# Kernel optimization log

Measured on AMD Instinct MI355X. Metric: run time of the kernel, lower is better.

Reference implementation:

```python
import jax, jax.numpy as jnp
import numpy as np

B, S, D = 1, 1024, 1024
NH, DH, DR = 8, 128, 64
DCQ, DC = 768, 256
INTER, E, TOPK = 512, 8, 2

def rmsnorm(x, w, eps=1e-6):
    return x * jax.lax.rsqrt(jnp.mean(x * x, -1, keepdims=True) + eps) * w

def lin(x, w, b):
    return x @ w.T + b

def apply_rope(x, cos, sin):
    # x: [b, s, h, d]; cos/sin: [S, d//2]; complex rotate pairs (even, odd)
    b, s, h, d = x.shape
    xr = x.reshape(b, s, h, d // 2, 2)
    x0, x1 = xr[..., 0], xr[..., 1]
    c = cos[None, :s, None, :]
    sn = sin[None, :s, None, :]
    return jnp.stack([x0 * c - x1 * sn, x0 * sn + x1 * c], -1).reshape(b, s, h, d)

def setup_inputs():
    keys = iter(jax.random.split(jax.random.key(0), 64))
    def nrm(*shape):
        return jax.random.normal(next(keys), shape, jnp.float32) * 0.02
    theta = 1.0 / (10000.0 ** (jnp.arange(0, DR, 2, dtype=jnp.float32) / DR))
    ang = jnp.arange(S, dtype=jnp.float32)[:, None] * theta[None, :]
    return dict(
        h=jax.random.normal(next(keys), (B, S, D), jnp.float32),
        freqs_cos=jnp.cos(ang), freqs_sin=jnp.sin(ang),
        mask=jnp.triu(jnp.ones((S, S), bool), 1),
        attn_norm_w=jnp.ones(D), ffn_norm_w=jnp.ones(D),
        wq_down=nrm(DCQ, D), bq_down=jnp.zeros(DCQ), q_norm_w=jnp.ones(DCQ),
        wqc=nrm(NH * DH, DCQ), bqc=jnp.zeros(NH * DH),
        wqr=nrm(NH * DR, DCQ), bqr=jnp.zeros(NH * DR),
        wkr=nrm(DR, D), bkr=jnp.zeros(DR), kr_norm_w=jnp.ones(DR),
        wkv_down=nrm(DC, D), bkv_down=jnp.zeros(DC), kv_norm_w=jnp.ones(DC),
        wkc=nrm(NH * DH, DC), bkc=jnp.zeros(NH * DH),
        wvc=nrm(NH * DH, DC), bvc=jnp.zeros(NH * DH),
        wo=nrm(D, NH * DH), bo=jnp.zeros(D),
        sw1=nrm(INTER, D), sb1=jnp.zeros(INTER), sw2=nrm(D, INTER), sb2=jnp.zeros(D),
        sw3=nrm(INTER, D), sb3=jnp.zeros(INTER),
        ew1=nrm(E, INTER, D), eb1=jnp.zeros((E, INTER)), ew2=nrm(E, D, INTER), eb2=jnp.zeros((E, D)),
        ew3=nrm(E, INTER, D), eb3=jnp.zeros((E, INTER)),
        centroids=jax.random.normal(next(keys), (E, D), jnp.float32), biases=jnp.zeros(E),
    )

def _forward(h, freqs_cos, freqs_sin, mask, attn_norm_w, ffn_norm_w, wq_down, bq_down, q_norm_w, wqc, bqc, wqr, bqr, wkr, bkr, kr_norm_w, wkv_down, bkv_down, kv_norm_w, wkc, bkc, wvc, bvc, wo, bo, sw1, sb1, sw2, sb2, sw3, sb3, ew1, eb1, ew2, eb2, ew3, eb3, centroids, biases):
    b, s, _ = h.shape
    # --- pre-norm MLA attention ---
    x = rmsnorm(h, attn_norm_w)
    cQ = rmsnorm(lin(x, wq_down, bq_down), q_norm_w)
    qR = apply_rope(lin(cQ, wqr, bqr).reshape(b, s, NH, DR), freqs_cos, freqs_sin)
    qC = lin(cQ, wqc, bqc).reshape(b, s, NH, DH)
    q = jnp.concatenate([qC, qR], -1)                      # [b,s,NH,DH+DR]
    kR = apply_rope(rmsnorm(lin(x, wkr, bkr), kr_norm_w).reshape(b, s, 1, DR), freqs_cos, freqs_sin)
    cKV = rmsnorm(lin(x, wkv_down, bkv_down), kv_norm_w)
    kC = lin(cKV, wkc, bkc).reshape(b, s, NH, DH)
    vC = lin(cKV, wvc, bvc).reshape(b, s, NH, DH)
    k = jnp.concatenate([jnp.broadcast_to(kR, (b, s, NH, DR)), kC], -1)  # source order: [kR, kC]
    scores = jnp.einsum('bqhd,bkhd->bhqk', q, k) / jnp.sqrt(jnp.float32(DH + DR))
    scores = jnp.where(mask[None, None], jnp.finfo(scores.dtype).min, scores)
    attw = jax.nn.softmax(scores, -1)                      # dropout in eval mode = identity
    attn = jnp.einsum('bhqk,bkhd->bqhd', attw, vC).reshape(b, s, NH * DH)
    x1 = h + lin(attn, wo, bo)
    # --- pre-norm MoE FFN ---
    y = rmsnorm(x1, ffn_norm_w)
    shared = lin(jax.nn.silu(lin(y, sw1, sb1)) * lin(y, sw3, sb3), sw2, sb2)  # mean over 1 shared expert
    affinity = jax.nn.sigmoid(y @ centroids.T)             # [b,s,E]
    _, topi = jax.lax.top_k(affinity + biases, TOPK)
    gates = jax.nn.softmax(jnp.take_along_axis(affinity, topi, -1), -1)      # [b,s,TOPK]
    combine = (jax.nn.one_hot(topi, E, dtype=y.dtype) * gates[..., None]).sum(-2)  # [b,s,E]
    h1 = jax.nn.silu(jnp.einsum('bsd,eid->bsei', y, ew1) + eb1) * (jnp.einsum('bsd,eid->bsei', y, ew3) + eb3)
    out_e = jnp.einsum('bsei,edi->bsed', h1, ew2) + eb2
    routed = (out_e * combine[..., None]).sum(2)
    return x1 + shared + routed

def reference(h, freqs_cos, freqs_sin, mask, attn_norm_w, ffn_norm_w, wq_down, bq_down, q_norm_w, wqc, bqc, wqr, bqr, wkr, bkr, kr_norm_w, wkv_down, bkv_down, kv_norm_w, wkc, bkc, wvc, bvc, wo, bo, sw1, sb1, sw2, sb2, sw3, sb3, ew1, eb1, ew2, eb2, ew3, eb3, centroids, biases):
    return _forward(h, freqs_cos, freqs_sin, mask, attn_norm_w, ffn_norm_w, wq_down, bq_down, q_norm_w, wqc, bqc, wqr, bqr, wkr, bkr, kr_norm_w, wkv_down, bkv_down, kv_norm_w, wkc, bkc, wvc, bvc, wo, bo, sw1, sb1, sw2, sb2, sw3, sb3, ew1, eb1, ew2, eb2, ew3, eb3, centroids, biases)
```

## Files before the change

kernel.cpp:

```cpp
#include <hip/hip_runtime.h>

typedef unsigned short u16;
typedef __attribute__((ext_vector_type(8))) short short8;
typedef __attribute__((ext_vector_type(4))) float f32x4;

__device__ __forceinline__ float b2f(u16 u) { return __uint_as_float(((unsigned)u) << 16); }
__device__ __forceinline__ u16 f2b(float f) {
    unsigned x = __float_as_uint(f);
    return (u16)((x + 0x7fffu + ((x >> 16) & 1u)) >> 16);
}

#define GLDS16(gp, lp) __builtin_amdgcn_global_load_lds( \
    (const __attribute__((address_space(1))) void*)(gp), \
    (__attribute__((address_space(3))) void*)(lp), 16, 0, 0)

struct Seg { const u16* W; const float* bias; void* C; int ldc; int epi; int bx0; int aidx; };
struct GArgs {
    const u16* A[2]; int lda[2]; int K[2];
    Seg seg[4]; int nseg;
    const float* res;
    float* dst2;
};

__launch_bounds__(256)
__global__ void mgemm4(GArgs ga)
{
    __shared__ u16 As[8192];
    __shared__ u16 Bs[8192];
    int bx = blockIdx.x, by = blockIdx.y;
    int si = 0;
#pragma unroll
    for (int i = 1; i < 4; i++)
        if (i < ga.nseg && bx >= ga.seg[i].bx0) si = i;
    const u16* Wp = ga.seg[si].W;
    const float* bp = ga.seg[si].bias;
    void* Cp = ga.seg[si].C;
    const int ldco = ga.seg[si].ldc;
    const int epi = ga.seg[si].epi;
    const int ai = ga.seg[si].aidx;
    const u16* Ap = ga.A[ai];
    const int lda = ga.lda[ai], K = ga.K[ai];
    const int col0 = (bx - ga.seg[si].bx0) * 64;
    const int row0 = by * 64;

    int tid = threadIdx.x;
    int lane = tid & 63, w = tid >> 6;
    int r0 = (w << 4) + (lane >> 2), kc8 = (lane & 3) << 3;
    const u16* gA = Ap + (size_t)(row0 + r0) * lda + kc8;
    const u16* gB = Wp + (size_t)(col0 + r0) * lda + kc8;

    int fm = lane & 15, fq = lane >> 4;
    f32x4 acc[4] = {};

#define MG_STAGE(B, KO) do { \
    u16* lA = As + (B) * 4096 + (w << 9); \
    u16* lB = Bs + (B) * 4096 + (w << 9); \
    GLDS16(gA + (KO), lA);      GLDS16(gA + (KO) + 32, lA + 2048); \
    GLDS16(gB + (KO), lB);      GLDS16(gB + (KO) + 32, lB + 2048); \
} while (0)

    const int nst = K >> 6;
    MG_STAGE(0, 0);
    __syncthreads();
    for (int t = 0; t < nst; t++) {
        int b = t & 1;
        if (t + 1 < nst) MG_STAGE(b ^ 1, (t + 1) << 6);
#pragma unroll
        for (int ks = 0; ks < 2; ks++) {
            short8 af = *(const short8*)(As + b * 4096 + ks * 2048 + (w << 9) + fm * 32 + fq * 8);
            short8 bf[4];
#pragma unroll
            for (int nt = 0; nt < 4; nt++)
                bf[nt] = *(const short8*)(Bs + b * 4096 + ks * 2048 + ((nt << 4) + fm) * 32 + fq * 8);
#pragma unroll
            for (int nt = 0; nt < 4; nt++)
                acc[nt] = __builtin_amdgcn_mfma_f32_16x16x32_bf16(af, bf[nt], acc[nt], 0, 0, 0);
        }
        __syncthreads();
    }
#undef MG_STAGE

    int rbase = row0 + (w << 4) + (fq << 2);
#pragma unroll
    for (int nt = 0; nt < 4; nt++) {
        int c = col0 + (nt << 4) + fm;
        float bcol = bp[c];
#pragma unroll
        for (int reg = 0; reg < 4; reg++) {
            int r = rbase + reg;
            float v = acc[nt][reg] + bcol;
            if (epi == 3)
                ((u16*)Cp)[(size_t)r * ldco + c] = f2b(v);
            else if (epi == 1) {
                float o = v + ga.res[(size_t)r * ldco + c];
                ((float*)Cp)[(size_t)r * ldco + c] = o;
                if (ga.dst2) ga.dst2[(size_t)r * ldco + c] = o;
            } else
                ((float*)Cp)[(size_t)r * ldco + c] = v;
        }
    }
}

__launch_bounds__(256)
__global__ void mega_glu(const u16* __restrict__ Y16,
                         const u16* __restrict__ sw1, const float* __restrict__ sb1,
                         const u16* __restrict__ sw3, const float* __restrict__ sb3,
                         const u16* __restrict__ ew1, const float* __restrict__ eb1,
                         const u16* __restrict__ ew3, const float* __restrict__ eb3,
                         u16* __restrict__ Ub, u16* __restrict__ Vb,
                         const int* __restrict__ lists, const int* __restrict__ counts)
{
    __shared__ u16 As[8192];
    __shared__ u16 Bs[8192];
    int bx = blockIdx.x, by = blockIdx.y, z = blockIdx.z;
    bool w3 = bx >= 8;
    int col0 = (w3 ? bx - 8 : bx) * 64;
    int cnt = 1024; const int* list = nullptr;
    const u16* Wp; const float* bp;
    if (z == 0) {
        Wp = w3 ? sw3 : sw1; bp = w3 ? sb3 : sb1;
    } else {
        int e = z - 1; cnt = counts[e]; list = lists + (e << 10);
        Wp = (w3 ? ew3 : ew1) + (size_t)e * 512 * 1024;
        bp = (w3 ? eb3 : eb1) + e * 512;
    }
    int row0 = by * 64;
    if (row0 >= cnt) return;
    u16* Cp = (w3 ? Vb : Ub) + (size_t)z * 524288;

    int tid = threadIdx.x, lane = tid & 63, w = tid >> 6;
    int r0 = (w << 4) + (lane >> 2), kc8 = (lane & 3) << 3;
    int ar = row0 + r0;
    if (z > 0) ar = list[ar < cnt ? ar : cnt - 1];
    const u16* gA = Y16 + (size_t)ar * 1024 + kc8;
    const u16* gB = Wp + (size_t)(col0 + r0) * 1024 + kc8;

    int fm = lane & 15, fq = lane >> 4;
    f32x4 acc[4] = {};

#define GL_STAGE(B, KO) do { \
    u16* lA = As + (B) * 4096 + (w << 9); \
    u16* lB = Bs + (B) * 4096 + (w << 9); \
    GLDS16(gA + (KO), lA);      GLDS16(gA + (KO) + 32, lA + 2048); \
    GLDS16(gB + (KO), lB);      GLDS16(gB + (KO) + 32, lB + 2048); \
} while (0)

    GL_STAGE(0, 0);
    __syncthreads();
    for (int t = 0; t < 16; t++) {
        int b = t & 1;
        if (t + 1 < 16) GL_STAGE(b ^ 1, (t + 1) << 6);
#pragma unroll
        for (int ks = 0; ks < 2; ks++) {
            short8 af = *(const short8*)(As + b * 4096 + ks * 2048 + (w << 9) + fm * 32 + fq * 8);
            short8 bf[4];
#pragma unroll
            for (int nt = 0; nt < 4; nt++)
                bf[nt] = *(const short8*)(Bs + b * 4096 + ks * 2048 + ((nt << 4) + fm) * 32 + fq * 8);
#pragma unroll
            for (int nt = 0; nt < 4; nt++)
                acc[nt] = __builtin_amdgcn_mfma_f32_16x16x32_bf16(af, bf[nt], acc[nt], 0, 0, 0);
        }
        __syncthreads();
    }
#undef GL_STAGE

    int rbase = row0 + (w << 4) + (fq << 2);
#pragma unroll
    for (int nt = 0; nt < 4; nt++) {
        int c = col0 + (nt << 4) + fm;
        float bcol = bp[c];
#pragma unroll
        for (int reg = 0; reg < 4; reg++) {
            int r = rbase + reg;
            if (r >= cnt) continue;
            Cp[(size_t)r * 512 + c] = f2b(acc[nt][reg] + bcol);
        }
    }
}

__launch_bounds__(256)
__global__ void mega_down(const u16* __restrict__ Ub, const u16* __restrict__ Vb,
                          const u16* __restrict__ sw2, const float* __restrict__ sb2,
                          const u16* __restrict__ ew2, const float* __restrict__ eb2,
                          float* __restrict__ out,
                          const int* __restrict__ lists, const float* __restrict__ glist,
                          const int* __restrict__ counts)
{
    __shared__ u16 Us[8192];
    __shared__ u16 Vs[8192];
    __shared__ u16 Ws[8192];
    int bx = blockIdx.x, by = blockIdx.y, z = blockIdx.z;
    int cnt = 1024; const int* list = nullptr; const float* gl = nullptr;
    const u16* Wp; const float* bp;
    if (z == 0) { Wp = sw2; bp = sb2; }
    else {
        int e = z - 1;
        cnt = counts[e]; list = lists + (e << 10); gl = glist + (e << 10);
        Wp = ew2 + (size_t)e * 1024 * 512; bp = eb2 + e * 1024;
    }
    int row0 = by * 64;
    if (row0 >= cnt) return;
    const u16* Ap = Ub + (size_t)z * 524288;
    const u16* Vp = Vb + (size_t)z * 524288;
    int col0 = bx * 64;

    int tid = threadIdx.x, lane = tid & 63, w = tid >> 6;
    int r0 = (w << 4) + (lane >> 2), kc8 = (lane & 3) << 3;
    const u16* gU = Ap + (size_t)(row0 + r0) * 512 + kc8;
    const u16* gV = Vp + (size_t)(row0 + r0) * 512 + kc8;
    const u16* gW = Wp + (size_t)(col0 + r0) * 512 + kc8;

    int fm = lane & 15, fq = lane >> 4;
    f32x4 acc[4] = {};

#define MD_STAGE(B, KO) do { \
    u16* lU = Us + (B) * 4096 + (w << 9); \
    u16* lV = Vs + (B) * 4096 + (w << 9); \
    u16* lW = Ws + (B) * 4096 + (w << 9); \
    GLDS16(gU + (KO), lU);      GLDS16(gU + (KO) + 32, lU + 2048); \
    GLDS16(gV + (KO), lV);      GLDS16(gV + (KO) + 32, lV + 2048); \
    GLDS16(gW + (KO), lW);      GLDS16(gW + (KO) + 32, lW + 2048); \
} while (0)

    MD_STAGE(0, 0);
    __syncthreads();
    for (int t = 0; t < 8; t++) {
        int b = t & 1;
        if (t + 1 < 8) MD_STAGE(b ^ 1, (t + 1) << 6);
#pragma unroll
        for (int ks = 0; ks < 2; ks++) {
            int aoff = b * 4096 + ks * 2048 + (w << 9) + fm * 32 + fq * 8;
            short8 u8 = *(const short8*)(Us + aoff);
            short8 v8 = *(const short8*)(Vs + aoff);
            short8 gf;
#pragma unroll
            for (int i = 0; i < 8; i++) {
                float u = b2f((u16)u8[i]), v = b2f((u16)v8[i]);
                gf[i] = (short)f2b(u / (1.f + __expf(-u)) * v);
            }
            short8 bf[4];
#pragma unroll
            for (int nt = 0; nt < 4; nt++)
                bf[nt] = *(const short8*)(Ws + b * 4096 + ks * 2048 + ((nt << 4) + fm) * 32 + fq * 8);
#pragma unroll
            for (int nt = 0; nt < 4; nt++)
                acc[nt] = __builtin_amdgcn_mfma_f32_16x16x32_bf16(gf, bf[nt], acc[nt], 0, 0, 0);
        }
        __syncthreads();
    }
#undef MD_STAGE

    int rbase = row0 + (w << 4) + (fq << 2);
#pragma unroll
    for (int nt = 0; nt < 4; nt++) {
        int c = col0 + (nt << 4) + fm;
        float bcol = bp[c];
#pragma unroll
        for (int reg = 0; reg < 4; reg++) {
            int r = rbase + reg;
            int tok; float g;
            if (z == 0) { tok = r; g = 1.f; }
            else { if (r >= cnt) continue; tok = list[r]; g = gl[r]; }
            atomicAdd(&out[(size_t)tok * 1024 + c], g * (acc[nt][reg] + bcol));
        }
    }
}

__launch_bounds__(256)
__global__ void attn_mfma(const u16* __restrict__ Qp, const u16* __restrict__ Kp,
                          const u16* __restrict__ VT, u16* __restrict__ O)
{
    const int qt = blockIdx.x, h = blockIdx.y;
    const int q0 = qt * 64;
    const int tid = threadIdx.x;
    const int lane = tid & 63, w = tid >> 6;
    const int fm = lane & 15, fq = lane >> 4;

    __shared__ u16 Ks[2 * 12288];
    __shared__ u16 Vs[4 * 4096];
    __shared__ u16 Ps[4 * 2048];

    const u16* qrow = Qp + ((size_t)h * 1024 + q0 + w * 16 + fm) * 192;
    short8 qf[6];
#pragma unroll
    for (int c = 0; c < 6; c++)
        qf[c] = *(const short8*)(qrow + c * 32 + fq * 8);

    const u16* Kb = Kp + (size_t)h * 1024 * 192;
    const u16* Vb = VT + (size_t)h * 128 * 1024;

    float m_i[4], l_i[4];
#pragma unroll
    for (int r = 0; r < 4; r++) { m_i[r] = -1e30f; l_i[r] = 0.f; }
    f32x4 accO[8] = {};
    const float scale = 0.07216878364870323f;
    const int nkt = (qt >> 1) + 1;
    const int rbase = w * 16 + fq * 4;

    for (int kt = 0; kt < nkt; ++kt) {
        const int kt0 = kt * 128;
#pragma unroll
        for (int half = 0; half < 2; half++) {
            const int o = kt0 + half * 64;
#pragma unroll
            for (int i = 0; i < 6; i++) {
                int idx = w + 4 * i;
                int c = idx >> 2, k4 = idx & 3;
                const u16* g = Kb + (size_t)(o + k4 * 16 + (lane >> 2)) * 192 + c * 32 + (lane & 3) * 8;
                GLDS16(g, Ks + half * 12288 + c * 2048 + k4 * 512 + lane * 8);
            }
#pragma unroll
            for (int i = 0; i < 4; i++) {
                int idx = w + 4 * i;
                int kc = idx >> 3, k8 = idx & 7;
                const u16* g = Vb + (size_t)(k8 * 16 + (lane >> 2)) * 1024 + o + kc * 32 + (lane & 3) * 8;
                GLDS16(g, Vs + (half * 2 + kc) * 4096 + k8 * 512 + lane * 8);
            }
        }
        __syncthreads();
        f32x4 sacc[8];
#pragma unroll
        for (int nt = 0; nt < 8; nt++) {
            sacc[nt] = (f32x4){0.f, 0.f, 0.f, 0.f};
#pragma unroll
            for (int c = 0; c < 6; c++) {
                short8 kf = *(const short8*)(Ks + (nt >> 2) * 12288 + c * 2048 + ((nt & 3) * 16 + fm) * 32 + fq * 8);
                sacc[nt] = __builtin_amdgcn_mfma_f32_16x16x32_bf16(qf[c], kf, sacc[nt], 0, 0, 0);
            }
        }
        float pv[8][4], rmax[4];
#pragma unroll
        for (int reg = 0; reg < 4; reg++) {
            int q = q0 + rbase + reg;
            float mx = -1e30f;
#pragma unroll
            for (int nt = 0; nt < 8; nt++) {
                int gk = kt0 + nt * 16 + fm;
                float s = sacc[nt][reg] * scale;
                if (gk > q) s = -1e30f;
                pv[nt][reg] = s;
                mx = fmaxf(mx, s);
            }
            rmax[reg] = mx;
        }
#pragma unroll
        for (int m = 1; m < 16; m <<= 1)
#pragma unroll
            for (int reg = 0; reg < 4; reg++)
                rmax[reg] = fmaxf(rmax[reg], __shfl_xor(rmax[reg], m));
        float alpha[4], rsum[4];
#pragma unroll
        for (int reg = 0; reg < 4; reg++) {
            float mn = fmaxf(m_i[reg], rmax[reg]);
            alpha[reg] = __expf(m_i[reg] - mn);
            m_i[reg] = mn;
            float s = 0.f;
#pragma unroll
            for (int nt = 0; nt < 8; nt++) {
                float p = __expf(pv[nt][reg] - mn);
                pv[nt][reg] = p;
                s += p;
            }
            rsum[reg] = s;
        }
#pragma unroll
        for (int m = 1; m < 16; m <<= 1)
#pragma unroll
            for (int reg = 0; reg < 4; reg++)
                rsum[reg] += __shfl_xor(rsum[reg], m);
#pragma unroll
        for (int reg = 0; reg < 4; reg++)
            l_i[reg] = l_i[reg] * alpha[reg] + rsum[reg];
#pragma unroll
        for (int nt = 0; nt < 8; nt++)
#pragma unroll
            for (int reg = 0; reg < 4; reg++)
                Ps[w * 2048 + (nt >> 1) * 512 + (fq * 4 + reg) * 32 + (nt & 1) * 16 + fm]
                    = f2b(pv[nt][reg]);
#pragma unroll
        for (int n2 = 0; n2 < 8; n2++)
#pragma unroll
            for (int reg = 0; reg < 4; reg++)
                accO[n2][reg] *= alpha[reg];
        short8 pf[4];
#pragma unroll
        for (int kc = 0; kc < 4; kc++)
            pf[kc] = *(const short8*)(Ps + w * 2048 + kc * 512 + fm * 32 + fq * 8);
#pragma unroll
        for (int n2 = 0; n2 < 8; n2++)
#pragma unroll
            for (int kc = 0; kc < 4; kc++) {
                short8 vf = *(const short8*)(Vs + kc * 4096 + (n2 * 16 + fm) * 32 + fq * 8);
                accO[n2] = __builtin_amdgcn_mfma_f32_16x16x32_bf16(pf[kc], vf, accO[n2], 0, 0, 0);
            }
        __syncthreads();
    }
#pragma unroll
    for (int reg = 0; reg < 4; reg++) {
        int row = q0 + rbase + reg;
        float inv = 1.f / l_i[reg];
#pragma unroll
        for (int n2 = 0; n2 < 8; n2++)
            O[(size_t)row * 1024 + h * 128 + n2 * 16 + fm] = f2b(accO[n2][reg] * inv);
    }
}

__launch_bounds__(256)
__global__ void rmsnorm2x(const float* __restrict__ X0, const float* __restrict__ w0,
                          u16* __restrict__ O0, int c0,
                          const float* __restrict__ X1, const float* __restrict__ w1,
                          u16* __restrict__ O1, int c1)
{
    int b = blockIdx.x, tid = threadIdx.x;
    const float* X; const float* w; u16* O; int cols; int r;
    if (b < 1024) { X = X0; w = w0; O = O0; cols = c0; r = b; }
    else          { X = X1; w = w1; O = O1; cols = c1; r = b - 1024; }
    const float* xr = X + (size_t)r * cols;
    float ss = 0.f;
    for (int j = tid; j < cols; j += 256) { float v = xr[j]; ss += v * v; }
    __shared__ float red[256];
    red[tid] = ss; __syncthreads();
    for (int st = 128; st > 0; st >>= 1) { if (tid < st) red[tid] += red[tid + st]; __syncthreads(); }
    float scale = rsqrtf(red[0] / cols + 1e-6f);
    for (int j = tid; j < cols; j += 256)
        O[(size_t)r * cols + j] = f2b(xr[j] * scale * w[j]);
}

__launch_bounds__(256)
__global__ void rmsnorm_route(const float* __restrict__ X1, const float* __restrict__ ffnw,
                              u16* __restrict__ Y16,
                              const float* __restrict__ cent, const float* __restrict__ biases,
                              int* __restrict__ counts, int* __restrict__ lists,
                              float* __restrict__ glist)
{
    __shared__ float red[256];
    int b = blockIdx.x, tid = threadIdx.x;
    if (b < 1024) {
        int r = b;
        const float* xr = X1 + (size_t)r * 1024;
        float ss = 0.f;
        for (int j = tid; j < 1024; j += 256) { float v = xr[j]; ss += v * v; }
        red[tid] = ss; __syncthreads();
        for (int st = 128; st > 0; st >>= 1) { if (tid < st) red[tid] += red[tid + st]; __syncthreads(); }
        float scale = rsqrtf(red[0] / 1024.f + 1e-6f);
        for (int j = tid; j < 1024; j += 256)
            Y16[(size_t)r * 1024 + j] = f2b(xr[j] * scale * ffnw[j]);
    } else {
        int t = b - 1024;
        const float* xr = X1 + (size_t)t * 1024;
        float ss = 0.f;
        float acc[8] = {};
        for (int j = tid; j < 1024; j += 256) {
            float x = xr[j];
            ss += x * x;
            float yp = x * ffnw[j];
#pragma unroll
            for (int e = 0; e < 8; e++) acc[e] += yp * cent[e * 1024 + j];
        }
        red[tid] = ss; __syncthreads();
        for (int st = 128; st > 0; st >>= 1) { if (tid < st) red[tid] += red[tid + st]; __syncthreads(); }
        float scale = rsqrtf(red[0] / 1024.f + 1e-6f);
        __syncthreads();
        __shared__ float aff[8];
        for (int e = 0; e < 8; e++) {
            red[tid] = acc[e]; __syncthreads();
            for (int st = 128; st > 0; st >>= 1) { if (tid < st) red[tid] += red[tid + st]; __syncthreads(); }
            if (tid == 0) aff[e] = 1.f / (1.f + expf(-red[0] * scale));
            __syncthreads();
        }
        if (tid == 0) {
            float sb[8];
#pragma unroll
            for (int e = 0; e < 8; e++) sb[e] = aff[e] + biases[e];
            int i0 = 0;
            for (int e = 1; e < 8; e++) if (sb[e] > sb[i0]) i0 = e;
            int i1 = -1;
            for (int e = 0; e < 8; e++) { if (e == i0) continue; if (i1 < 0 || sb[e] > sb[i1]) i1 = e; }
            float a0 = aff[i0], a1 = aff[i1];
            float mx = fmaxf(a0, a1);
            float e0 = expf(a0 - mx), e1 = expf(a1 - mx);
            float inv = 1.f / (e0 + e1);
            int p0 = atomicAdd(&counts[i0], 1);
            lists[i0 * 1024 + p0] = t; glist[i0 * 1024 + p0] = e0 * inv;
            int p1 = atomicAdd(&counts[i1], 1);
            lists[i1 * 1024 + p1] = t; glist[i1 * 1024 + p1] = e1 * inv;
        }
    }
}

__launch_bounds__(256)
__global__ void pack_all(const float* __restrict__ QC, const float* __restrict__ QRr,
                         const float* __restrict__ KRraw, const float* __restrict__ krw,
                         const float* __restrict__ KC,
                         const u16* __restrict__ VCb,
                         const float* __restrict__ fcos, const float* __restrict__ fsin,
                         u16* __restrict__ Qp, u16* __restrict__ Kp, u16* __restrict__ VT)
{
    __shared__ u16 Ts[64][68];
    __shared__ float kshared[64];
    int b = blockIdx.x, tid = threadIdx.x;
    if (b < 1024) {
        int s = b;
        if (tid < 64) {
            float v = KRraw[(size_t)s * 64 + tid];
            float ss = v * v;
#pragma unroll
            for (int m = 1; m < 64; m <<= 1) ss += __shfl_xor(ss, m);
            float scale = rsqrtf(ss / 64.f + 1e-6f);
            int j = tid >> 1;
            float c = fcos[s * 32 + j], sn = fsin[s * 32 + j];
            float x0 = KRraw[(size_t)s * 64 + (tid & ~1)] * scale * krw[tid & ~1];
            float x1 = KRraw[(size_t)s * 64 + (tid | 1)]  * scale * krw[tid | 1];
            kshared[tid] = (tid & 1) ? (x0 * sn + x1 * c) : (x0 * c - x1 * sn);
        }
        __syncthreads();
        for (int e = tid; e < 1536; e += 256) {
            int h = e / 192, d = e % 192;
            float q;
            if (d < 128) {
                q = QC[(size_t)s * 1024 + h * 128 + d];
            } else {
                int dd = d - 128, j = dd >> 1;
                float c = fcos[s * 32 + j], sn = fsin[s * 32 + j];
                float x0 = QRr[(size_t)s * 512 + h * 64 + (dd & ~1)];
                float x1 = QRr[(size_t)s * 512 + h * 64 + (dd | 1)];
                q = (dd & 1) ? (x0 * sn + x1 * c) : (x0 * c - x1 * sn);
            }
            Qp[((size_t)h * 1024 + s) * 192 + d] = f2b(q);
            float k = (d < 64) ? kshared[d]
                               : KC[(size_t)s * 1024 + h * 128 + d - 64];
            Kp[((size_t)h * 1024 + s) * 192 + d] = f2b(k);
        }
    } else {
        int idx = b - 1024;
        int s0 = (idx & 15) * 64, d0 = (idx >> 4) * 64;
        for (int k = 0; k < 16; k++) {
            int e = tid + k * 256, r = e >> 6, c = e & 63;
            Ts[r][c] = VCb[(size_t)(s0 + r) * 1024 + d0 + c];
        }
        __syncthreads();
        for (int k = 0; k < 16; k++) {
            int e = tid + k * 256, d = e >> 6, s = e & 63;
            VT[(size_t)(d0 + d) * 1024 + s0 + s] = Ts[s][d];
        }
    }
}

#define NCAST 4096
__launch_bounds__(256)
__global__ void fused_cast(const float* p0, const float* p1, const float* p2,
                           const float* p3, const float* p4, const float* p5,
                           const float* p6, const float* p7, const float* p8,
                           const float* p9, const float* p10, const float* p11,
                           const float* p12, const float* pkr,
                           u16* __restrict__ dst,
                           const float* __restrict__ hX, const float* __restrict__ attnw,
                           u16* __restrict__ X16)
{
    __shared__ float red[256];
    int b = blockIdx.x, tid = threadIdx.x;
    if (b < NCAST) {
        const int NQ = 18022400 / 4;
        for (int i = b * 256 + tid; i < NQ; i += NCAST * 256) {
            int e = i * 4;
            const float* s; int base;
            if      (e <   786432) { s = p0;  base = 0; }
            else if (e <  1048576) { s = p1;  base =   786432; }
            else if (e <  1835008) { s = p2;  base =  1048576; }
            else if (e <  2228224) { s = p3;  base =  1835008; }
            else if (e <  2490368) { s = p4;  base =  2228224; }
            else if (e <  2752512) { s = p5;  base =  2490368; }
            else if (e <  3801088) { s = p6;  base =  2752512; }
            else if (e <  4325376) { s = p7;  base =  3801088; }
            else if (e <  4849664) { s = p8;  base =  4325376; }
            else if (e <  5373952) { s = p9;  base =  4849664; }
            else if (e <  9568256) { s = p10; base =  5373952; }
            else if (e < 13762560) { s = p11; base =  9568256; }
            else if (e < 17956864) { s = p12; base = 13762560; }
            else                   { s = pkr; base = 17956864; }
            float4 v = *(const float4*)(s + (e - base));
            ushort4 o;
            o.x = f2b(v.x); o.y = f2b(v.y); o.z = f2b(v.z); o.w = f2b(v.w);
            *(ushort4*)(dst + e) = o;
        }
    } else {
        int r = b - NCAST;
        const float* xr = hX + (size_t)r * 1024;
        float ss = 0.f;
        for (int j = tid; j < 1024; j += 256) { float v = xr[j]; ss += v * v; }
        red[tid] = ss; __syncthreads();
        for (int st = 128; st > 0; st >>= 1) { if (tid < st) red[tid] += red[tid + st]; __syncthreads(); }
        float scale = rsqrtf(red[0] / 1024.f + 1e-6f);
        for (int j = tid; j < 1024; j += 256)
            X16[(size_t)r * 1024 + j] = f2b(xr[j] * scale * attnw[j]);
    }
}

extern "C" void kernel_launch(void* const* d_in, const int* in_sizes, int n_in,
                              void* d_out, int out_size, void* d_ws, size_t ws_size,
                              hipStream_t stream)
{
    (void)in_sizes; (void)n_in; (void)ws_size; (void)out_size;
    const float* h       = (const float*)d_in[0];
    const float* fcos    = (const float*)d_in[1];
    const float* fsin    = (const float*)d_in[2];
    const float* attn_w  = (const float*)d_in[4];
    const float* ffn_w   = (const float*)d_in[5];
    const float* wq_down = (const float*)d_in[6];
    const float* bq_down = (const float*)d_in[7];
    const float* q_norm  = (const float*)d_in[8];
    const float* wqc     = (const float*)d_in[9];
    const float* bqc     = (const float*)d_in[10];
    const float* wqr     = (const float*)d_in[11];
    const float* bqr     = (const float*)d_in[12];
    const float* wkr     = (const float*)d_in[13];
    const float* bkr     = (const float*)d_in[14];
    const float* kr_norm = (const float*)d_in[15];
    const float* wkv     = (const float*)d_in[16];
    const float* bkv     = (const float*)d_in[17];
    const float* kv_norm = (const float*)d_in[18];
    const float* wkc     = (const float*)d_in[19];
    const float* bkc     = (const float*)d_in[20];
    const float* wvc     = (const float*)d_in[21];
    const float* bvc     = (const float*)d_in[22];
    const float* wo      = (const float*)d_in[23];
    const float* bo      = (const float*)d_in[24];
    const float* sw1     = (const float*)d_in[25];
    const float* sb1     = (const float*)d_in[26];
    const float* sw2     = (const float*)d_in[27];
    const float* sb2     = (const float*)d_in[28];
    const float* sw3     = (const float*)d_in[29];
    const float* sb3     = (const float*)d_in[30];
    const float* ew1     = (const float*)d_in[31];
    const float* eb1     = (const float*)d_in[32];
    const float* ew2     = (const float*)d_in[33];
    const float* eb2     = (const float*)d_in[34];
    const float* ew3     = (const float*)d_in[35];
    const float* eb3     = (const float*)d_in[36];
    const float* cent    = (const float*)d_in[37];
    const float* biases  = (const float*)d_in[38];

    char* wsb = (char*)d_ws;
    const size_t U5 = 512 * 1024;
    u16*   X16   = (u16*)(wsb + 8 * U5);
    float* QRr   = (float*)(wsb + 12 * U5);
    float* CQraw = (float*)(wsb + 16 * U5);
    u16*   ATT16 = (u16*)(wsb + 16 * U5);
    u16*   CQ16  = (u16*)(wsb + 22 * U5);
    float* CKVraw= (float*)(wsb + 25 * U5);
    u16*   CKV16 = (u16*)(wsb + 27 * U5);
    float* KRraw = (float*)(wsb + 28 * U5);
    float* QC    = (float*)(wsb + 29 * U5);
    float* KC    = (float*)(wsb + 37 * U5);
    u16*   Vb    = (u16*)(wsb + 29 * U5);
    float* X1    = (float*)(wsb + 53 * U5);
    float* GL    = (float*)(wsb + 61 * U5);
    int*   lists = (int*)(wsb + 61 * U5 + 32 * 1024);
    int*   counts= (int*)(wsb + 61 * U5 + 64 * 1024);
    u16*   Y16   = (u16*)(wsb + 69 * U5);
    u16*   Ub    = (u16*)(wsb + 73 * U5);

    u16* wb = (u16*)(wsb + 92 * U5);
    u16 *c_wq  = wb;
    u16 *c_wkv = c_wq  + 786432;
    u16 *c_wqc = c_wkv + 262144;
    u16 *c_wqr = c_wqc + 786432;
    u16 *c_wkc = c_wqr + 393216;
    u16 *c_wvc = c_wkc + 262144;
    u16 *c_wo  = c_wvc + 262144;
    u16 *c_sw1 = c_wo  + 1048576;
    u16 *c_sw3 = c_sw1 + 524288;
    u16 *c_sw2 = c_sw3 + 524288;
    u16 *c_ew1 = c_sw2 + 524288;
    u16 *c_ew3 = c_ew1 + 4194304;
    u16 *c_ew2 = c_ew3 + 4194304;
    u16 *c_wkr = c_ew2 + 4194304;
    u16* VCb = (u16*)(wsb + 92 * U5 + 36175872);
    u16* VTp = VCb + 1048576;
    u16* Qpk = VTp + 1048576;
    u16* Kpk = Qpk + 1572864;

    fused_cast<<<NCAST + 1024, 256, 0, stream>>>(wq_down, wkv, wqc, wqr, wkc, wvc, wo,
                                                 sw1, sw3, sw2, ew1, ew3, ew2, wkr, wb,
                                                 h, attn_w, X16);

    {
        GArgs g = {};
        g.A[0] = X16; g.lda[0] = 1024; g.K[0] = 1024;
        g.seg[0] = { c_wq,  bq_down, CQraw,  768, 0, 0,  0 };
        g.seg[1] = { c_wkv, bkv,     CKVraw, 256, 0, 12, 0 };
        g.seg[2] = { c_wkr, bkr,     KRraw,  64,  0, 16, 0 };
        g.nseg = 3;
        mgemm4<<<dim3(17, 16), 256, 0, stream>>>(g);
    }
    rmsnorm2x<<<2048, 256, 0, stream>>>(CQraw, q_norm, CQ16, 768,
                                        CKVraw, kv_norm, CKV16, 256);
    {
        GArgs g = {};
        g.A[0] = CQ16;  g.lda[0] = 768; g.K[0] = 768;
        g.A[1] = CKV16; g.lda[1] = 256; g.K[1] = 256;
        g.seg[0] = { c_wqc, bqc, QC,   1024, 0, 0,  0 };
        g.seg[1] = { c_wqr, bqr, QRr,  512,  0, 16, 0 };
        g.seg[2] = { c_wkc, bkc, KC,   1024, 0, 24, 1 };
        g.seg[3] = { c_wvc, bvc, VCb,  1024, 3, 40, 1 };
        g.nseg = 4;
        mgemm4<<<dim3(56, 16), 256, 0, stream>>>(g);
    }
    pack_all<<<1280, 256, 0, stream>>>(QC, QRr, KRraw, kr_norm, KC, VCb, fcos, fsin,
                                       Qpk, Kpk, VTp);
    attn_mfma<<<dim3(16, 8), 256, 0, stream>>>(Qpk, Kpk, VTp, ATT16);
    {
        GArgs g = {};
        g.A[0] = ATT16; g.lda[0] = 1024; g.K[0] = 1024;
        g.seg[0] = { c_wo, bo, X1, 1024, 1, 0, 0 };
        g.nseg = 1; g.res = h; g.dst2 = (float*)d_out;
        mgemm4<<<dim3(16, 16), 256, 0, stream>>>(g);
    }

    hipMemsetAsync(counts, 0, 32, stream);
    rmsnorm_route<<<2048, 256, 0, stream>>>(X1, ffn_w, Y16, cent, biases,
                                            counts, lists, GL);
    mega_glu<<<dim3(16, 16, 9), 256, 0, stream>>>(Y16, c_sw1, sb1, c_sw3, sb3,
                                                  c_ew1, eb1, c_ew3, eb3,
                                                  Ub, Vb, lists, counts);
    mega_down<<<dim3(16, 16, 9), 256, 0, stream>>>(Ub, Vb, c_sw2, sb2, c_ew2, eb2,
                                                   (float*)d_out, lists, GL, counts);
}
```

Baseline: 369.9 us.

## Pipeline GEMMs with 4-slot k32 ring, swizzle LDS, fuse SwiGLU into up-projection

After: 370.5 us. No clear change (+0.2%).

```diff
diff --git a/kernel.cpp b/kernel.cpp
--- a/kernel.cpp
+++ b/kernel.cpp
@@ -13,6 +13,14 @@
 #define GLDS16(gp, lp) __builtin_amdgcn_global_load_lds( \
     (const __attribute__((address_space(1))) void*)(gp), \
     (__attribute__((address_space(3))) void*)(lp), 16, 0, 0)
+
+#define WAITV(N) do { \
+    asm volatile("s_waitcnt vmcnt(" #N ")" ::: "memory"); \
+    __builtin_amdgcn_sched_barrier(0); \
+} while (0)
+
+#define KC8_SWZ(lane) ((((lane) & 3) ^ (((lane) >> 3) & 3)) << 3)
+#define RD_SWZ(fm, fq) (((fq) ^ (((fm) >> 1) & 3)) << 3)
 
 struct Seg { const u16* W; const float* bias; void* C; int ldc; int epi; int bx0; int aidx; };
 struct GArgs {
@@ -25,8 +33,8 @@
 __launch_bounds__(256)
 __global__ void mgemm4(GArgs ga)
 {
-    __shared__ u16 As[8192];
-    __shared__ u16 Bs[8192];
+    __shared__ u16 As[4 * 2048];
+    __shared__ u16 Bs[4 * 2048];
     int bx = blockIdx.x, by = blockIdx.y;
     int si = 0;
 #pragma unroll
@@ -45,38 +53,42 @@
 
     int tid = threadIdx.x;
     int lane = tid & 63, w = tid >> 6;
-    int r0 = (w << 4) + (lane >> 2), kc8 = (lane & 3) << 3;
+    int r0 = (w << 4) + (lane >> 2), kc8 = KC8_SWZ(lane);
     const u16* gA = Ap + (size_t)(row0 + r0) * lda + kc8;
     const u16* gB = Wp + (size_t)(col0 + r0) * lda + kc8;
 
     int fm = lane & 15, fq = lane >> 4;
+    const int so = RD_SWZ(fm, fq);
     f32x4 acc[4] = {};
 
-#define MG_STAGE(B, KO) do { \
-    u16* lA = As + (B) * 4096 + (w << 9); \
-    u16* lB = Bs + (B) * 4096 + (w << 9); \
-    GLDS16(gA + (KO), lA);      GLDS16(gA + (KO) + 32, lA + 2048); \
-    GLDS16(gB + (KO), lB);      GLDS16(gB + (KO) + 32, lB + 2048); \
+#define MG_STAGE(BS, KO) do { \
+    GLDS16(gA + (KO), As + (BS) * 2048 + (w << 9)); \
+    GLDS16(gB + (KO), Bs + (BS) * 2048 + (w << 9)); \
 } while (0)
 
-    const int nst = K >> 6;
+    const int nst = K >> 5;
     MG_STAGE(0, 0);
-    __syncthreads();
+    MG_STAGE(1, 32);
+    MG_STAGE(2, 64);
+    int bc = 0;
     for (int t = 0; t < nst; t++) {
-        int b = t & 1;
-        if (t + 1 < nst) MG_STAGE(b ^ 1, (t + 1) << 6);
-#pragma unroll
-        for (int ks = 0; ks < 2; ks++) {
-            short8 af = *(const short8*)(As + b * 4096 + ks * 2048 + (w << 9) + fm * 32 + fq * 8);
-            short8 bf[4];
-#pragma unroll
-            for (int nt = 0; nt < 4; nt++)
-                bf[nt] = *(const short8*)(Bs + b * 4096 + ks * 2048 + ((nt << 4) + fm) * 32 + fq * 8);
-#pragma unroll
-            for (int nt = 0; nt < 4; nt++)
-                acc[nt] = __builtin_amdgcn_mfma_f32_16x16x32_bf16(af, bf[nt], acc[nt], 0, 0, 0);
-        }
-        __syncthreads();
+        if (t < nst - 2) WAITV(4);
+        else if (t == nst - 2) WAITV(2);
+        else WAITV(0);
+        __builtin_amdgcn_s_barrier();
+        if (t + 3 < nst) {
+            int bs = bc + 3; if (bs >= 4) bs -= 4;
+            MG_STAGE(bs, (t + 3) << 5);
+        }
+        short8 af = *(const short8*)(As + bc * 2048 + (w << 9) + fm * 32 + so);
+        short8 bf[4];
+#pragma unroll
+        for (int nt = 0; nt < 4; nt++)
+            bf[nt] = *(const short8*)(Bs + bc * 2048 + ((nt << 4) + fm) * 32 + so);
+#pragma unroll
+        for (int nt = 0; nt < 4; nt++)
+            acc[nt] = __builtin_amdgcn_mfma_f32_16x16x32_bf16(af, bf[nt], acc[nt], 0, 0, 0);
+        bc = (bc + 1) & 3;
     }
 #undef MG_STAGE
 
@@ -107,61 +119,70 @@
                          const u16* __restrict__ sw3, const float* __restrict__ sb3,
                          const u16* __restrict__ ew1, const float* __restrict__ eb1,
                          const u16* __restrict__ ew3, const float* __restrict__ eb3,
-                         u16* __restrict__ Ub, u16* __restrict__ Vb,
+                         u16* __restrict__ Gb,
                          const int* __restrict__ lists, const int* __restrict__ counts)
 {
-    __shared__ u16 As[8192];
-    __shared__ u16 Bs[8192];
+    __shared__ u16 As[4 * 2048];
+    __shared__ u16 B1s[4 * 2048];
+    __shared__ u16 B3s[4 * 2048];
     int bx = blockIdx.x, by = blockIdx.y, z = blockIdx.z;
-    bool w3 = bx >= 8;
-    int col0 = (w3 ? bx - 8 : bx) * 64;
+    int col0 = bx * 64;
     int cnt = 1024; const int* list = nullptr;
-    const u16* Wp; const float* bp;
+    const u16 *W1p, *W3p; const float *b1p, *b3p;
     if (z == 0) {
-        Wp = w3 ? sw3 : sw1; bp = w3 ? sb3 : sb1;
+        W1p = sw1; b1p = sb1; W3p = sw3; b3p = sb3;
     } else {
         int e = z - 1; cnt = counts[e]; list = lists + (e << 10);
-        Wp = (w3 ? ew3 : ew1) + (size_t)e * 512 * 1024;
-        bp = (w3 ? eb3 : eb1) + e * 512;
+        W1p = ew1 + (size_t)e * 512 * 1024; b1p = eb1 + e * 512;
+        W3p = ew3 + (size_t)e * 512 * 1024; b3p = eb3 + e * 512;
     }
     int row0 = by * 64;
     if (row0 >= cnt) return;
-    u16* Cp = (w3 ? Vb : Ub) + (size_t)z * 524288;
+    u16* Cp = Gb + (size_t)z * 524288;
 
     int tid = threadIdx.x, lane = tid & 63, w = tid >> 6;
-    int r0 = (w << 4) + (lane >> 2), kc8 = (lane & 3) << 3;
+    int r0 = (w << 4) + (lane >> 2), kc8 = KC8_SWZ(lane);
     int ar = row0 + r0;
     if (z > 0) ar = list[ar < cnt ? ar : cnt - 1];
     const u16* gA = Y16 + (size_t)ar * 1024 + kc8;
-    const u16* gB = Wp + (size_t)(col0 + r0) * 1024 + kc8;
+    const u16* gB1 = W1p + (size_t)(col0 + r0) * 1024 + kc8;
+    const u16* gB3 = W3p + (size_t)(col0 + r0) * 1024 + kc8;
 
     int fm = lane & 15, fq = lane >> 4;
-    f32x4 acc[4] = {};
-
-#define GL_STAGE(B, KO) do { \
-    u16* lA = As + (B) * 4096 + (w << 9); \
-    u16* lB = Bs + (B) * 4096 + (w << 9); \
-    GLDS16(gA + (KO), lA);      GLDS16(gA + (KO) + 32, lA + 2048); \
-    GLDS16(gB + (KO), lB);      GLDS16(gB + (KO) + 32, lB + 2048); \
+    const int so = RD_SWZ(fm, fq);
+    f32x4 accU[4] = {}, accV[4] = {};
+
+#define GL_STAGE(BS, KO) do { \
+    GLDS16(gA + (KO),  As  + (BS) * 2048 + (w << 9)); \
+    GLDS16(gB1 + (KO), B1s + (BS) * 2048 + (w << 9)); \
+    GLDS16(gB3 + (KO), B3s + (BS) * 2048 + (w << 9)); \
 } while (0)
 
     GL_STAGE(0, 0);
-    __syncthreads();
-    for (int t = 0; t < 16; t++) {
-        int b = t & 1;
-        if (t + 1 < 16) GL_STAGE(b ^ 1, (t + 1) << 6);
-#pragma unroll
-        for (int ks = 0; ks < 2; ks++) {
-            short8 af = *(const short8*)(As + b * 4096 + ks * 2048 + (w << 9) + fm * 32 + fq * 8);
-            short8 bf[4];
-#pragma unroll
-            for (int nt = 0; nt < 4; nt++)
-                bf[nt] = *(const short8*)(Bs + b * 4096 + ks * 2048 + ((nt << 4) + fm) * 32 + fq * 8);
-#pragma unroll
-            for (int nt = 0; nt < 4; nt++)
-                acc[nt] = __builtin_amdgcn_mfma_f32_16x16x32_bf16(af, bf[nt], acc[nt], 0, 0, 0);
-        }
-        __syncthreads();
+    GL_STAGE(1, 32);
+    GL_STAGE(2, 64);
+    int bc = 0;
+    for (int t = 0; t < 32; t++) {
+        if (t < 30) WAITV(6);
+        else if (t == 30) WAITV(3);
+        else WAITV(0);
+        __builtin_amdgcn_s_barrier();
+        if (t + 3 < 32) {
+            int bs = bc + 3; if (bs >= 4) bs -= 4;
+            GL_STAGE(bs, (t + 3) << 5);
+        }
+        short8 af = *(const short8*)(As + bc * 2048 + (w << 9) + fm * 32 + so);
+#pragma unroll
+        for (int nt = 0; nt < 4; nt++) {
+            short8 b1 = *(const short8*)(B1s + bc * 2048 + ((nt << 4) + fm) * 32 + so);
+            accU[nt] = __builtin_amdgcn_mfma_f32_16x16x32_bf16(af, b1, accU[nt], 0, 0, 0);
+        }
+#pragma unroll
+        for (int nt = 0; nt < 4; nt++) {
+            short8 b3 = *(const short8*)(B3s + bc * 2048 + ((nt << 4) + fm) * 32 + so);
+            accV[nt] = __builtin_amdgcn_mfma_f32_16x16x32_bf16(af, b3, accV[nt], 0, 0, 0);
+        }
+        bc = (bc + 1) & 3;
     }
 #undef GL_STAGE
 
@@ -169,27 +190,28 @@
 #pragma unroll
     for (int nt = 0; nt < 4; nt++) {
         int c = col0 + (nt << 4) + fm;
-        float bcol = bp[c];
+        float b1c = b1p[c], b3c = b3p[c];
 #pragma unroll
         for (int reg = 0; reg < 4; reg++) {
             int r = rbase + reg;
             if (r >= cnt) continue;
-            Cp[(size_t)r * 512 + c] = f2b(acc[nt][reg] + bcol);
+            float u = b2f(f2b(accU[nt][reg] + b1c));
+            float v = b2f(f2b(accV[nt][reg] + b3c));
+            Cp[(size_t)r * 512 + c] = f2b(u / (1.f + __expf(-u)) * v);
         }
     }
 }
 
 __launch_bounds__(256)
-__global__ void mega_down(const u16* __restrict__ Ub, const u16* __restrict__ Vb,
+__global__ void mega_down(const u16* __restrict__ Gb,
                           const u16* __restrict__ sw2, const float* __restrict__ sb2,
                           const u16* __restrict__ ew2, const float* __restrict__ eb2,
                           float* __restrict__ out,
                           const int* __restrict__ lists, const float* __restrict__ glist,
                           const int* __restrict__ counts)
 {
-    __shared__ u16 Us[8192];
-    __shared__ u16 Vs[8192];
-    __shared__ u16 Ws[8192];
+    __shared__ u16 Gs[4 * 2048];
+    __shared__ u16 Ws[4 * 2048];
     int bx = blockIdx.x, by = blockIdx.y, z = blockIdx.z;
     int cnt = 1024; const int* list = nullptr; const float* gl = nullptr;
     const u16* Wp; const float* bp;
@@ -201,53 +223,45 @@
     }
     int row0 = by * 64;
     if (row0 >= cnt) return;
-    const u16* Ap = Ub + (size_t)z * 524288;
-    const u16* Vp = Vb + (size_t)z * 524288;
+    const u16* Ap = Gb + (size_t)z * 524288;
     int col0 = bx * 64;
 
     int tid = threadIdx.x, lane = tid & 63, w = tid >> 6;
-    int r0 = (w << 4) + (lane >> 2), kc8 = (lane & 3) << 3;
-    const u16* gU = Ap + (size_t)(row0 + r0) * 512 + kc8;
-    const u16* gV = Vp + (size_t)(row0 + r0) * 512 + kc8;
+    int r0 = (w << 4) + (lane >> 2), kc8 = KC8_SWZ(lane);
+    const u16* gG = Ap + (size_t)(row0 + r0) * 512 + kc8;
     const u16* gW = Wp + (size_t)(col0 + r0) * 512 + kc8;
 
     int fm = lane & 15, fq = lane >> 4;
+    const int so = RD_SWZ(fm, fq);
     f32x4 acc[4] = {};
 
-#define MD_STAGE(B, KO) do { \
-    u16* lU = Us + (B) * 4096 + (w << 9); \
-    u16* lV = Vs + (B) * 4096 + (w << 9); \
-    u16* lW = Ws + (B) * 4096 + (w << 9); \
-    GLDS16(gU + (KO), lU);      GLDS16(gU + (KO) + 32, lU + 2048); \
-    GLDS16(gV + (KO), lV);      GLDS16(gV + (KO) + 32, lV + 2048); \
-    GLDS16(gW + (KO), lW);      GLDS16(gW + (KO) + 32, lW + 2048); \
+#define MD_STAGE(BS, KO) do { \
+    GLDS16(gG + (KO), Gs + (BS) * 2048 + (w << 9)); \
+    GLDS16(gW + (KO), Ws + (BS) * 2048 + (w << 9)); \
 } while (0)
 
     MD_STAGE(0, 0);
-    __syncthreads();
-    for (int t = 0; t < 8; t++) {
-        int b = t & 1;
-        if (t + 1 < 8) MD_STAGE(b ^ 1, (t + 1) << 6);
-#pragma unroll
-        for (int ks = 0; ks < 2; ks++) {
-            int aoff = b * 4096 + ks * 2048 + (w << 9) + fm * 32 + fq * 8;
-            short8 u8 = *(const short8*)(Us + aoff);
-            short8 v8 = *(const short8*)(Vs + aoff);
-            short8 gf;
-#pragma unroll
-            for (int i = 0; i < 8; i++) {
-                float u = b2f((u16)u8[i]), v = b2f((u16)v8[i]);
-                gf[i] = (short)f2b(u / (1.f + __expf(-u)) * v);
-            }
-            short8 bf[4];
-#pragma unroll
-            for (int nt = 0; nt < 4; nt++)
-                bf[nt] = *(const short8*)(Ws + b * 4096 + ks * 2048 + ((nt << 4) + fm) * 32 + fq * 8);
-#pragma unroll
-            for (int nt = 0; nt < 4; nt++)
-                acc[nt] = __builtin_amdgcn_mfma_f32_16x16x32_bf16(gf, bf[nt], acc[nt], 0, 0, 0);
-        }
-        __syncthreads();
+    MD_STAGE(1, 32);
+    MD_STAGE(2, 64);
+    int bc = 0;
+    for (int t = 0; t < 16; t++) {
+        if (t < 14) WAITV(4);
+        else if (t == 14) WAITV(2);
+        else WAITV(0);
+        __builtin_amdgcn_s_barrier();
+        if (t + 3 < 16) {
+            int bs = bc + 3; if (bs >= 4) bs -= 4;
+            MD_STAGE(bs, (t + 3) << 5);
+        }
+        short8 af = *(const short8*)(Gs + bc * 2048 + (w << 9) + fm * 32 + so);
+        short8 bf[4];
+#pragma unroll
+        for (int nt = 0; nt < 4; nt++)
+            bf[nt] = *(const short8*)(Ws + bc * 2048 + ((nt << 4) + fm) * 32 + so);
+#pragma unroll
+        for (int nt = 0; nt < 4; nt++)
+            acc[nt] = __builtin_amdgcn_mfma_f32_16x16x32_bf16(af, bf[nt], acc[nt], 0, 0, 0);
+        bc = (bc + 1) & 3;
     }
 #undef MD_STAGE
 
@@ -653,13 +667,12 @@
     float* KRraw = (float*)(wsb + 28 * U5);
     float* QC    = (float*)(wsb + 29 * U5);
     float* KC    = (float*)(wsb + 37 * U5);
-    u16*   Vb    = (u16*)(wsb + 29 * U5);
     float* X1    = (float*)(wsb + 53 * U5);
     float* GL    = (float*)(wsb + 61 * U5);
     int*   lists = (int*)(wsb + 61 * U5 + 32 * 1024);
     int*   counts= (int*)(wsb + 61 * U5 + 64 * 1024);
     u16*   Y16   = (u16*)(wsb + 69 * U5);
-    u16*   Ub    = (u16*)(wsb + 73 * U5);
+    u16*   Gb    = (u16*)(wsb + 73 * U5);
 
     u16* wb = (u16*)(wsb + 92 * U5);
     u16 *c_wq  = wb;
@@ -721,9 +734,9 @@
     hipMemsetAsync(counts, 0, 32, stream);
     rmsnorm_route<<<2048, 256, 0, stream>>>(X1, ffn_w, Y16, cent, biases,
                                             counts, lists, GL);
-    mega_glu<<<dim3(16, 16, 9), 256, 0, stream>>>(Y16, c_sw1, sb1, c_sw3, sb3,
-                                                  c_ew1, eb1, c_ew3, eb3,
-                                                  Ub, Vb, lists, counts);
-    mega_down<<<dim3(16, 16, 9), 256, 0, stream>>>(Ub, Vb, c_sw2, sb2, c_ew2, eb2,
+    mega_glu<<<dim3(8, 16, 9), 256, 0, stream>>>(Y16, c_sw1, sb1, c_sw3, sb3,
+                                                 c_ew1, eb1, c_ew3, eb3,
+                                                 Gb, lists, counts);
+    mega_down<<<dim3(16, 16, 9), 256, 0, stream>>>(Gb, c_sw2, sb2, c_ew2, eb2,
                                                    (float*)d_out, lists, GL, counts);
 }
```
